# Performance work log

Hardware: AMD Instinct MI355X
Metric: run time of the kernel (lower is better)

Reference implementation:

```python
import jax, jax.numpy as jnp
import numpy as np

B, S, D, H = 8, 1024, 512, 8
HD = D // H
EPS = 1e-5


def layer_norm(x, g, b):
    m = jnp.mean(x, axis=-1, keepdims=True)
    v = jnp.mean(jnp.square(x - m), axis=-1, keepdims=True)
    return (x - m) * jax.lax.rsqrt(v + EPS) * g + b


def mha(x, w_in, b_in, w_out, b_out):
    # x: [B,S,D]; w_in: [3D,D]; PyTorch MultiheadAttention math (no dropout, eval)
    b, s, d = x.shape
    qkv = x @ w_in.T + b_in                      # [B,S,3D]
    q, k, v = jnp.split(qkv, 3, axis=-1)
    q = q.reshape(b, s, H, HD)
    k = k.reshape(b, s, H, HD)
    v = v.reshape(b, s, H, HD)
    scores = jnp.einsum('bqhd,bkhd->bhqk', q, k) / np.sqrt(HD)
    a = jax.nn.softmax(scores, axis=-1)
    o = jnp.einsum('bhqk,bkhd->bqhd', a, v).reshape(b, s, d)
    return o @ w_out.T + b_out


def interp_linear(y, out_size):
    # y: [B,S_in,D]; torch F.interpolate(mode='linear', align_corners=False)
    s_in = y.shape[1]
    scale = s_in / out_size
    src = (jnp.arange(out_size, dtype=jnp.float32) + 0.5) * scale - 0.5
    src = jnp.clip(src, 0.0, s_in - 1.0)
    i0 = jnp.floor(src).astype(jnp.int32)
    i1 = jnp.minimum(i0 + 1, s_in - 1)
    w = (src - i0.astype(jnp.float32))[None, :, None]
    return y[:, i0, :] * (1.0 - w) + y[:, i1, :] * w


def setup_inputs() -> dict:
    key = jax.random.key(0)
    ks = jax.random.split(key, 16)
    sd = 0.02
    return {
        'x': jax.random.normal(ks[0], (B, S, D), jnp.float32),
        'w_in1': jax.random.normal(ks[1], (3 * D, D), jnp.float32) * sd,
        'b_in1': jnp.zeros((3 * D,), jnp.float32),
        'w_out1': jax.random.normal(ks[2], (D, D), jnp.float32) * sd,
        'b_out1': jnp.zeros((D,), jnp.float32),
        'w_in2': jax.random.normal(ks[3], (3 * D, D), jnp.float32) * sd,
        'b_in2': jnp.zeros((3 * D,), jnp.float32),
        'w_out2': jax.random.normal(ks[4], (D, D), jnp.float32) * sd,
        'b_out2': jnp.zeros((D,), jnp.float32),
        'g1': jnp.ones((D,), jnp.float32), 'beta1': jnp.zeros((D,), jnp.float32),
        'g2': jnp.ones((D,), jnp.float32), 'beta2': jnp.zeros((D,), jnp.float32),
        'g3': jnp.ones((D,), jnp.float32), 'beta3': jnp.zeros((D,), jnp.float32),
        'w_ff1': jax.random.normal(ks[5], (4 * D, D), jnp.float32) * sd,
        'b_ff1': jnp.zeros((4 * D,), jnp.float32),
        'w_ff2': jax.random.normal(ks[6], (D, 4 * D), jnp.float32) * sd,
        'b_ff2': jnp.zeros((D,), jnp.float32),
    }


def reference(x, w_in1, b_in1, w_out1, b_out1, w_in2, b_in2, w_out2, b_out2,
              g1, beta1, g2, beta2, g3, beta3, w_ff1, b_ff1, w_ff2, b_ff2):
    a1 = mha(x, w_in1, b_in1, w_out1, b_out1)
    x = layer_norm(x + a1, g1, beta1)
    # avg_pool1d kernel=2 stride=2 ceil_mode (S even -> exact halving)
    pooled = x.reshape(B, S // 2, 2, D).mean(axis=2)
    a2 = mha(pooled, w_in2, b_in2, w_out2, b_out2)
    up = interp_linear(a2, S)
    x = layer_norm(x + up, g2, beta2)
    h = jax.nn.gelu(x @ w_ff1.T + b_ff1, approximate=False)
    ff = h @ w_ff2.T + b_ff2
    return layer_norm(x + ff, g3, beta3)
```

## Files before the change

kernel.cpp:

```cpp
#include <hip/hip_runtime.h>
#include <hip/hip_bf16.h>
#include <math.h>

typedef __hip_bfloat16 bf16;
typedef __attribute__((ext_vector_type(8))) short short8;
typedef __attribute__((ext_vector_type(4))) float f32x4;

__device__ __forceinline__ float ldf(const float* p, size_t i) { return p[i]; }
__device__ __forceinline__ float ldf(const bf16*  p, size_t i) { return __bfloat162float(p[i]); }
__device__ __forceinline__ void  stf(float* p, size_t i, float v) { p[i] = v; }
__device__ __forceinline__ void  stf(bf16*  p, size_t i, float v) { p[i] = __float2bfloat16(v); }

__global__ __launch_bounds__(256) void cvt_kernel(
    const float* __restrict__ src, bf16* __restrict__ dst, int n)
{
    for (int i = blockIdx.x * 256 + threadIdx.x; i < n; i += gridDim.x * 256)
        dst[i] = __float2bfloat16(src[i]);
}

template <int EPI>
__global__ __launch_bounds__(256) void gemm_mfma(
    const bf16* __restrict__ A, const bf16* __restrict__ W,
    const float* __restrict__ bias, bf16* __restrict__ C,
    int M, int N, int K)
{
    constexpr int LP = 72;
    __shared__ __align__(16) bf16 Asl[128 * LP];
    __shared__ __align__(16) bf16 Bsl[128 * LP];

    const int tid  = threadIdx.x;
    const int lane = tid & 63;
    const int wave = tid >> 6;
    const int wm   = wave >> 1;
    const int wn   = wave & 1;
    const int l15  = lane & 15;
    const int quad = lane >> 4;

    const int row0 = blockIdx.y * 128, col0 = blockIdx.x * 128;

    f32x4 acc[4][4] = {};

    for (int k0 = 0; k0 < K; k0 += 64) {
        #pragma unroll
        for (int t = 0; t < 4; t++) {
            int chunk = tid + 256 * t;
            int r = chunk >> 3, c = (chunk & 7) * 8;
            *(short8*)&Asl[r * LP + c] =
                *(const short8*)&A[(size_t)(row0 + r) * K + k0 + c];
            *(short8*)&Bsl[r * LP + c] =
                *(const short8*)&W[(size_t)(col0 + r) * K + k0 + c];
        }
        __syncthreads();

        #pragma unroll
        for (int ks = 0; ks < 64; ks += 32) {
            short8 af[4], bfr[4];
            #pragma unroll
            for (int mt = 0; mt < 4; mt++)
                af[mt] = *(const short8*)&Asl[(wm * 64 + mt * 16 + l15) * LP + ks + quad * 8];
            #pragma unroll
            for (int nt = 0; nt < 4; nt++)
                bfr[nt] = *(const short8*)&Bsl[(wn * 64 + nt * 16 + l15) * LP + ks + quad * 8];
            #pragma unroll
            for (int mt = 0; mt < 4; mt++)
                #pragma unroll
                for (int nt = 0; nt < 4; nt++)
                    acc[mt][nt] = __builtin_amdgcn_mfma_f32_16x16x32_bf16(
                        af[mt], bfr[nt], acc[mt][nt], 0, 0, 0);
        }
        __syncthreads();
    }

    #pragma unroll
    for (int mt = 0; mt < 4; mt++) {
        int row = row0 + wm * 64 + mt * 16 + quad * 4;
        #pragma unroll
        for (int nt = 0; nt < 4; nt++) {
            int col = col0 + wn * 64 + nt * 16 + l15;
            float bv = bias[col];
            #pragma unroll
            for (int r = 0; r < 4; r++) {
                float v = acc[mt][nt][r] + bv;
                if (EPI == 1) v = 0.5f * v * (1.0f + erff(v * 0.70710678118654752f));
                C[(size_t)(row + r) * N + col] = __float2bfloat16(v);
            }
        }
    }
}

__global__ __launch_bounds__(256) void flash_attn_mfma(
    const bf16* __restrict__ qkv, bf16* __restrict__ o, int S)
{
    __shared__ __align__(16) bf16 Ks[64 * 72];
    __shared__ __align__(16) bf16 Vt[64 * 68];
    __shared__ __align__(16) bf16 Pl[4][16 * 72];
    __shared__ float aX[4][16];

    const int tid = threadIdx.x;
    const int wave = tid >> 6, lane = tid & 63;
    const int l15 = lane & 15, quad = lane >> 4;
    const int q0 = blockIdx.x * 64, h = blockIdx.y, bb = blockIdx.z;
    const bf16* base = qkv + (size_t)bb * S * 1536 + h * 64;

    const size_t qoff = (size_t)(q0 + wave * 16 + l15) * 1536;
    short8 qf0 = *(const short8*)&base[qoff + quad * 8];
    short8 qf1 = *(const short8*)&base[qoff + 32 + quad * 8];

    f32x4 oacc[4] = {};
    float mrow = -3.0e38f, lrow = 0.f;

    for (int k0 = 0; k0 < S; k0 += 64) {
        __syncthreads();

        #pragma unroll
        for (int t = 0; t < 2; t++) {
            int c = tid + 256 * t;
            int r = c >> 3, col = (c & 7) * 8;
            *(short8*)&Ks[r * 72 + col] =
                *(const short8*)&base[(size_t)(k0 + r) * 1536 + 512 + col];
        }
        #pragma unroll
        for (int i = 0; i < 16; i++) {
            int r = i * 4 + wave;
            Vt[lane * 68 + r] = base[(size_t)(k0 + r) * 1536 + 1024 + lane];
        }
        __syncthreads();

        f32x4 st[4] = {};
        #pragma unroll
        for (int mt = 0; mt < 4; mt++) {
            short8 kf0 = *(const short8*)&Ks[(mt * 16 + l15) * 72 + quad * 8];
            short8 kf1 = *(const short8*)&Ks[(mt * 16 + l15) * 72 + 32 + quad * 8];
            st[mt] = __builtin_amdgcn_mfma_f32_16x16x32_bf16(kf0, qf0, st[mt], 0, 0, 0);
            st[mt] = __builtin_amdgcn_mfma_f32_16x16x32_bf16(kf1, qf1, st[mt], 0, 0, 0);
        }

        float cm = -3.0e38f;
        #pragma unroll
        for (int mt = 0; mt < 4; mt++)
            #pragma unroll
            for (int r = 0; r < 4; r++) {
                st[mt][r] *= 0.125f;
                cm = fmaxf(cm, st[mt][r]);
            }
        cm = fmaxf(cm, __shfl_xor(cm, 16));
        cm = fmaxf(cm, __shfl_xor(cm, 32));
        float mn = fmaxf(mrow, cm);
        float alpha = __expf(mrow - mn);
        mrow = mn;

        float ps = 0.f;
        #pragma unroll
        for (int mt = 0; mt < 4; mt++)
            #pragma unroll
            for (int r = 0; r < 4; r++) {
                float p = __expf(st[mt][r] - mn);
                ps += p;
                Pl[wave][l15 * 72 + mt * 16 + quad * 4 + r] = __float2bfloat16(p);
            }
        ps += __shfl_xor(ps, 16);
        ps += __shfl_xor(ps, 32);
        lrow = lrow * alpha + ps;

        if (quad == 0) aX[wave][l15] = alpha;
        float a4[4];
        #pragma unroll
        for (int r = 0; r < 4; r++) a4[r] = aX[wave][quad * 4 + r];
        #pragma unroll
        for (int nt = 0; nt < 4; nt++)
            #pragma unroll
            for (int r = 0; r < 4; r++) oacc[nt][r] *= a4[r];

        #pragma unroll
        for (int kb = 0; kb < 2; kb++) {
            short8 pf = *(const short8*)&Pl[wave][l15 * 72 + kb * 32 + quad * 8];
            #pragma unroll
            for (int nt = 0; nt < 4; nt++) {
                const bf16* vp = &Vt[(nt * 16 + l15) * 68 + kb * 32 + quad * 8];
                short8 vf;
                *(long*)&vf = *(const long*)vp;
                *((long*)&vf + 1) = *(const long*)(vp + 4);
                oacc[nt] = __builtin_amdgcn_mfma_f32_16x16x32_bf16(pf, vf, oacc[nt], 0, 0, 0);
            }
        }
    }

    if (quad == 0) aX[wave][l15] = 1.0f / lrow;
    float iv[4];
    #pragma unroll
    for (int r = 0; r < 4; r++) iv[r] = aX[wave][quad * 4 + r];

    #pragma unroll
    for (int nt = 0; nt < 4; nt++)
        #pragma unroll
        for (int r = 0; r < 4; r++) {
            size_t row = (size_t)bb * S + q0 + wave * 16 + quad * 4 + r;
            o[row * 512 + h * 64 + nt * 16 + l15] = __float2bfloat16(oacc[nt][r] * iv[r]);
        }
}

template <typename AT, typename OT, bool INTERP>
__global__ __launch_bounds__(256) void ln_kernel(
    const AT* __restrict__ a, const bf16* __restrict__ bsrc,
    const float* __restrict__ g, const float* __restrict__ beta,
    OT* __restrict__ out)
{
    const int row = blockIdx.x;
    const int t = threadIdx.x;
    const size_t base = (size_t)row * 512;

    float a0 = ldf(a, base + t), a1 = ldf(a, base + t + 256);
    float b0, b1;
    if (INTERP) {
        int s = row & 1023, bb = row >> 10;
        float src = fminf(fmaxf((s + 0.5f) * 0.5f - 0.5f, 0.f), 511.f);
        int i0 = (int)src;
        int i1 = min(i0 + 1, 511);
        float w = src - (float)i0;
        size_t r0 = ((size_t)bb * 512 + i0) * 512;
        size_t r1 = ((size_t)bb * 512 + i1) * 512;
        b0 = __bfloat162float(bsrc[r0 + t]) * (1.f - w) + __bfloat162float(bsrc[r1 + t]) * w;
        b1 = __bfloat162float(bsrc[r0 + t + 256]) * (1.f - w) + __bfloat162float(bsrc[r1 + t + 256]) * w;
    } else {
        b0 = __bfloat162float(bsrc[base + t]);
        b1 = __bfloat162float(bsrc[base + t + 256]);
    }
    float v0 = a0 + b0, v1 = a1 + b1;

    __shared__ float red[4];
    const int lane = t & 63, wid = t >> 6;

    float sm = v0 + v1;
    #pragma unroll
    for (int off = 32; off > 0; off >>= 1) sm += __shfl_xor(sm, off);
    if (lane == 0) red[wid] = sm;
    __syncthreads();
    sm = red[0] + red[1] + red[2] + red[3];
    const float mean = sm * (1.0f / 512.0f);

    float d0 = v0 - mean, d1 = v1 - mean;
    float vv = d0 * d0 + d1 * d1;
    __syncthreads();
    #pragma unroll
    for (int off = 32; off > 0; off >>= 1) vv += __shfl_xor(vv, off);
    if (lane == 0) red[wid] = vv;
    __syncthreads();
    vv = red[0] + red[1] + red[2] + red[3];
    const float rstd = rsqrtf(vv * (1.0f / 512.0f) + 1e-5f);

    stf(out, base + t,       d0 * rstd * g[t]       + beta[t]);
    stf(out, base + t + 256, d1 * rstd * g[t + 256] + beta[t + 256]);
}

__global__ __launch_bounds__(256) void pool_kernel(
    const bf16* __restrict__ x, bf16* __restrict__ p)
{
    size_t i = (size_t)blockIdx.x * 256 + threadIdx.x;
    size_t d = i & 511;
    size_t rs = i >> 9;
    size_t b = rs >> 9, s = rs & 511;
    size_t r = (b * 1024 + 2 * s) * 512 + d;
    p[i] = __float2bfloat16(0.5f * (__bfloat162float(x[r]) + __bfloat162float(x[r + 512])));
}

extern "C" void kernel_launch(void* const* d_in, const int* in_sizes, int n_in,
                              void* d_out, int out_size, void* d_ws, size_t ws_size,
                              hipStream_t stream)
{
    const float* x      = (const float*)d_in[0];
    const float* w_in1  = (const float*)d_in[1];
    const float* b_in1  = (const float*)d_in[2];
    const float* w_out1 = (const float*)d_in[3];
    const float* b_out1 = (const float*)d_in[4];
    const float* w_in2  = (const float*)d_in[5];
    const float* b_in2  = (const float*)d_in[6];
    const float* w_out2 = (const float*)d_in[7];
    const float* b_out2 = (const float*)d_in[8];
    const float* g1     = (const float*)d_in[9];
    const float* be1    = (const float*)d_in[10];
    const float* g2     = (const float*)d_in[11];
    const float* be2    = (const float*)d_in[12];
    const float* g3     = (const float*)d_in[13];
    const float* be3    = (const float*)d_in[14];
    const float* w_ff1  = (const float*)d_in[15];
    const float* b_ff1  = (const float*)d_in[16];
    const float* w_ff2  = (const float*)d_in[17];
    const float* b_ff2  = (const float*)d_in[18];

    bf16* ws     = (bf16*)d_ws;
    bf16* xb     = ws + 0;
    bf16* wq1    = ws + 4194304;
    bf16* wo1    = ws + 4980736;
    bf16* wq2    = ws + 5242880;
    bf16* wo2    = ws + 6029312;
    bf16* wf1    = ws + 6291456;
    bf16* wf2    = ws + 7340032;
    bf16* qkv1   = ws + 8388608;
    bf16* o1     = ws + 20971520;
    bf16* a1     = ws + 25165824;
    bf16* x1     = ws + 29360128;
    bf16* pooled = ws + 33554432;
    bf16* qkv2   = ws + 35651584;
    bf16* o2     = ws + 41943040;
    bf16* a2     = ws + 44040192;
    bf16* x2     = ws + 46137344;
    bf16* h      = ws + 8388608;
    bf16* ff     = ws + 25165824;

    dim3 blk(256);

    cvt_kernel<<<1024, blk, 0, stream>>>(x, xb, 4194304);
    cvt_kernel<<<512, blk, 0, stream>>>(w_in1, wq1, 786432);
    cvt_kernel<<<256, blk, 0, stream>>>(w_out1, wo1, 262144);
    cvt_kernel<<<512, blk, 0, stream>>>(w_in2, wq2, 786432);
    cvt_kernel<<<256, blk, 0, stream>>>(w_out2, wo2, 262144);
    cvt_kernel<<<512, blk, 0, stream>>>(w_ff1, wf1, 1048576);
    cvt_kernel<<<512, blk, 0, stream>>>(w_ff2, wf2, 1048576);

    gemm_mfma<0><<<dim3(12, 64), blk, 0, stream>>>(xb, wq1, b_in1, qkv1, 8192, 1536, 512);
    flash_attn_mfma<<<dim3(16, 8, 8), blk, 0, stream>>>(qkv1, o1, 1024);
    gemm_mfma<0><<<dim3(4, 64), blk, 0, stream>>>(o1, wo1, b_out1, a1, 8192, 512, 512);
    ln_kernel<float, bf16, false><<<8192, blk, 0, stream>>>(x, a1, g1, be1, x1);
    pool_kernel<<<8192, blk, 0, stream>>>(x1, pooled);
    gemm_mfma<0><<<dim3(12, 32), blk, 0, stream>>>(pooled, wq2, b_in2, qkv2, 4096, 1536, 512);
    flash_attn_mfma<<<dim3(8, 8, 8), blk, 0, stream>>>(qkv2, o2, 512);
    gemm_mfma<0><<<dim3(4, 32), blk, 0, stream>>>(o2, wo2, b_out2, a2, 4096, 512, 512);
    ln_kernel<bf16, bf16, true><<<8192, blk, 0, stream>>>(x1, a2, g2, be2, x2);
    gemm_mfma<1><<<dim3(16, 64), blk, 0, stream>>>(x2, wf1, b_ff1, h, 8192, 2048, 512);
    gemm_mfma<0><<<dim3(4, 64), blk, 0, stream>>>(h, wf2, b_ff2, ff, 8192, 512, 2048);
    ln_kernel<bf16, float, false><<<8192, blk, 0, stream>>>(x2, ff, g3, be3, (float*)d_out);
}
```

Baseline: 370.0 us.

## Use direct global-to-LDS loads in GEMM, multi-tile flash attention, fuse weight conversions

The GEMM now loads A/W tiles straight into shared memory with global_load_lds, drops the LDS row padding and moves the barrier to the top of the loop. Flash attention is templated to process two 16-row Q tiles per wave, reusing K/V fragments across them, and switches to exp2 with a folded scale, packed V transpose stores and vectorized P writes. The six weight conversions are merged into one launch. The unpadded LDS layout may cause bank conflicts on the MFMA fragment reads, and the larger attention tile halves the grid for the first attention.

```diff
diff --git a/kernel.cpp b/kernel.cpp
--- a/kernel.cpp
+++ b/kernel.cpp
@@ -4,6 +4,7 @@
 
 typedef __hip_bfloat16 bf16;
 typedef __attribute__((ext_vector_type(8))) short short8;
+typedef __attribute__((ext_vector_type(4))) short s4v;
 typedef __attribute__((ext_vector_type(4))) float f32x4;
 
 __device__ __forceinline__ float ldf(const float* p, size_t i) { return p[i]; }
@@ -11,11 +12,36 @@
 __device__ __forceinline__ void  stf(float* p, size_t i, float v) { p[i] = v; }
 __device__ __forceinline__ void  stf(bf16*  p, size_t i, float v) { p[i] = __float2bfloat16(v); }
 
+__device__ __forceinline__ float ex2(float x) { return __builtin_amdgcn_exp2f(x); }
+
+__device__ __forceinline__ void gl16(const void* gp, void* lp) {
+    __builtin_amdgcn_global_load_lds(
+        (const __attribute__((address_space(1))) void*)gp,
+        (__attribute__((address_space(3))) void*)lp, 16, 0, 0);
+}
+
 __global__ __launch_bounds__(256) void cvt_kernel(
     const float* __restrict__ src, bf16* __restrict__ dst, int n)
 {
     for (int i = blockIdx.x * 256 + threadIdx.x; i < n; i += gridDim.x * 256)
         dst[i] = __float2bfloat16(src[i]);
+}
+
+__global__ __launch_bounds__(256) void cvt_w(
+    const float* __restrict__ s0, const float* __restrict__ s1,
+    const float* __restrict__ s2, const float* __restrict__ s3,
+    const float* __restrict__ s4, const float* __restrict__ s5,
+    bf16* __restrict__ dst)
+{
+    int i = blockIdx.x * 256 + threadIdx.x;
+    const float* s; int off;
+    if      (i <  786432) { s = s0; off = 0; }
+    else if (i < 1048576) { s = s1; off =  786432; }
+    else if (i < 1835008) { s = s2; off = 1048576; }
+    else if (i < 2097152) { s = s3; off = 1835008; }
+    else if (i < 3145728) { s = s4; off = 2097152; }
+    else                  { s = s5; off = 3145728; }
+    dst[i] = __float2bfloat16(s[i - off]);
 }
 
 template <int EPI>
@@ -24,9 +50,8 @@
     const float* __restrict__ bias, bf16* __restrict__ C,
     int M, int N, int K)
 {
-    constexpr int LP = 72;
-    __shared__ __align__(16) bf16 Asl[128 * LP];
-    __shared__ __align__(16) bf16 Bsl[128 * LP];
+    __shared__ __align__(16) bf16 Asl[128 * 64];
+    __shared__ __align__(16) bf16 Bsl[128 * 64];
 
     const int tid  = threadIdx.x;
     const int lane = tid & 63;
@@ -35,20 +60,21 @@
     const int wn   = wave & 1;
     const int l15  = lane & 15;
     const int quad = lane >> 4;
+    const int sr   = lane >> 3;
+    const int sc   = (lane & 7) * 8;
 
     const int row0 = blockIdx.y * 128, col0 = blockIdx.x * 128;
 
     f32x4 acc[4][4] = {};
 
     for (int k0 = 0; k0 < K; k0 += 64) {
+        __syncthreads();
         #pragma unroll
         for (int t = 0; t < 4; t++) {
-            int chunk = tid + 256 * t;
-            int r = chunk >> 3, c = (chunk & 7) * 8;
-            *(short8*)&Asl[r * LP + c] =
-                *(const short8*)&A[(size_t)(row0 + r) * K + k0 + c];
-            *(short8*)&Bsl[r * LP + c] =
-                *(const short8*)&W[(size_t)(col0 + r) * K + k0 + c];
+            int r0 = wave * 32 + t * 8;
+            int r  = r0 + sr;
+            gl16(&A[(size_t)(row0 + r) * K + k0 + sc], &Asl[r0 * 64]);
+            gl16(&W[(size_t)(col0 + r) * K + k0 + sc], &Bsl[r0 * 64]);
         }
         __syncthreads();
 
@@ -57,10 +83,10 @@
             short8 af[4], bfr[4];
             #pragma unroll
             for (int mt = 0; mt < 4; mt++)
-                af[mt] = *(const short8*)&Asl[(wm * 64 + mt * 16 + l15) * LP + ks + quad * 8];
+                af[mt] = *(const short8*)&Asl[(wm * 64 + mt * 16 + l15) * 64 + ks + quad * 8];
             #pragma unroll
             for (int nt = 0; nt < 4; nt++)
-                bfr[nt] = *(const short8*)&Bsl[(wn * 64 + nt * 16 + l15) * LP + ks + quad * 8];
+                bfr[nt] = *(const short8*)&Bsl[(wn * 64 + nt * 16 + l15) * 64 + ks + quad * 8];
             #pragma unroll
             for (int mt = 0; mt < 4; mt++)
                 #pragma unroll
@@ -68,7 +94,6 @@
                     acc[mt][nt] = __builtin_amdgcn_mfma_f32_16x16x32_bf16(
                         af[mt], bfr[nt], acc[mt][nt], 0, 0, 0);
         }
-        __syncthreads();
     }
 
     #pragma unroll
@@ -88,26 +113,35 @@
     }
 }
 
+template <int NS>
 __global__ __launch_bounds__(256) void flash_attn_mfma(
     const bf16* __restrict__ qkv, bf16* __restrict__ o, int S)
 {
     __shared__ __align__(16) bf16 Ks[64 * 72];
     __shared__ __align__(16) bf16 Vt[64 * 68];
-    __shared__ __align__(16) bf16 Pl[4][16 * 72];
-    __shared__ float aX[4][16];
+    __shared__ __align__(16) bf16 Pl[4][NS * 16 * 72];
+    __shared__ float aX[4][NS * 16];
 
     const int tid = threadIdx.x;
     const int wave = tid >> 6, lane = tid & 63;
     const int l15 = lane & 15, quad = lane >> 4;
-    const int q0 = blockIdx.x * 64, h = blockIdx.y, bb = blockIdx.z;
+    const int q0 = blockIdx.x * (64 * NS), h = blockIdx.y, bb = blockIdx.z;
     const bf16* base = qkv + (size_t)bb * S * 1536 + h * 64;
 
-    const size_t qoff = (size_t)(q0 + wave * 16 + l15) * 1536;
-    short8 qf0 = *(const short8*)&base[qoff + quad * 8];
-    short8 qf1 = *(const short8*)&base[qoff + 32 + quad * 8];
-
-    f32x4 oacc[4] = {};
-    float mrow = -3.0e38f, lrow = 0.f;
+    short8 qf[NS][2];
+    #pragma unroll
+    for (int s = 0; s < NS; s++) {
+        size_t qoff = (size_t)(q0 + (wave * NS + s) * 16 + l15) * 1536;
+        qf[s][0] = *(const short8*)&base[qoff + quad * 8];
+        qf[s][1] = *(const short8*)&base[qoff + 32 + quad * 8];
+    }
+
+    f32x4 oacc[NS][4] = {};
+    float mrow[NS], lrow[NS];
+    #pragma unroll
+    for (int s = 0; s < NS; s++) { mrow[s] = -3.0e38f; lrow[s] = 0.f; }
+
+    const float CE = 0.18033688f;
 
     for (int k0 = 0; k0 < S; k0 += 64) {
         __syncthreads();
@@ -120,83 +154,106 @@
                 *(const short8*)&base[(size_t)(k0 + r) * 1536 + 512 + col];
         }
         #pragma unroll
-        for (int i = 0; i < 16; i++) {
-            int r = i * 4 + wave;
-            Vt[lane * 68 + r] = base[(size_t)(k0 + r) * 1536 + 1024 + lane];
+        for (int i = 0; i < 8; i++) {
+            int r = (wave * 8 + i) * 2;
+            union { bf16 b[2]; unsigned u; } pk;
+            pk.b[0] = base[(size_t)(k0 + r) * 1536 + 1024 + lane];
+            pk.b[1] = base[(size_t)(k0 + r + 1) * 1536 + 1024 + lane];
+            *(unsigned*)&Vt[lane * 68 + r] = pk.u;
         }
         __syncthreads();
 
-        f32x4 st[4] = {};
+        f32x4 st[NS][4] = {};
         #pragma unroll
         for (int mt = 0; mt < 4; mt++) {
             short8 kf0 = *(const short8*)&Ks[(mt * 16 + l15) * 72 + quad * 8];
             short8 kf1 = *(const short8*)&Ks[(mt * 16 + l15) * 72 + 32 + quad * 8];
-            st[mt] = __builtin_amdgcn_mfma_f32_16x16x32_bf16(kf0, qf0, st[mt], 0, 0, 0);
-            st[mt] = __builtin_amdgcn_mfma_f32_16x16x32_bf16(kf1, qf1, st[mt], 0, 0, 0);
-        }
-
-        float cm = -3.0e38f;
-        #pragma unroll
-        for (int mt = 0; mt < 4; mt++)
-            #pragma unroll
-            for (int r = 0; r < 4; r++) {
-                st[mt][r] *= 0.125f;
-                cm = fmaxf(cm, st[mt][r]);
-            }
-        cm = fmaxf(cm, __shfl_xor(cm, 16));
-        cm = fmaxf(cm, __shfl_xor(cm, 32));
-        float mn = fmaxf(mrow, cm);
-        float alpha = __expf(mrow - mn);
-        mrow = mn;
-
-        float ps = 0.f;
-        #pragma unroll
-        for (int mt = 0; mt < 4; mt++)
-            #pragma unroll
-            for (int r = 0; r < 4; r++) {
-                float p = __expf(st[mt][r] - mn);
-                ps += p;
-                Pl[wave][l15 * 72 + mt * 16 + quad * 4 + r] = __float2bfloat16(p);
-            }
-        ps += __shfl_xor(ps, 16);
-        ps += __shfl_xor(ps, 32);
-        lrow = lrow * alpha + ps;
-
-        if (quad == 0) aX[wave][l15] = alpha;
-        float a4[4];
-        #pragma unroll
-        for (int r = 0; r < 4; r++) a4[r] = aX[wave][quad * 4 + r];
-        #pragma unroll
-        for (int nt = 0; nt < 4; nt++)
-            #pragma unroll
-            for (int r = 0; r < 4; r++) oacc[nt][r] *= a4[r];
+            #pragma unroll
+            for (int s = 0; s < NS; s++) {
+                st[s][mt] = __builtin_amdgcn_mfma_f32_16x16x32_bf16(kf0, qf[s][0], st[s][mt], 0, 0, 0);
+                st[s][mt] = __builtin_amdgcn_mfma_f32_16x16x32_bf16(kf1, qf[s][1], st[s][mt], 0, 0, 0);
+            }
+        }
+
+        #pragma unroll
+        for (int s = 0; s < NS; s++) {
+            float cm = -3.0e38f;
+            #pragma unroll
+            for (int mt = 0; mt < 4; mt++)
+                #pragma unroll
+                for (int r = 0; r < 4; r++) cm = fmaxf(cm, st[s][mt][r]);
+            cm = fmaxf(cm, __shfl_xor(cm, 16));
+            cm = fmaxf(cm, __shfl_xor(cm, 32));
+            float mn = fmaxf(mrow[s], cm);
+            float alpha = ex2((mrow[s] - mn) * CE);
+            mrow[s] = mn;
+            float mb = mn * CE;
+            float ps = 0.f;
+            #pragma unroll
+            for (int mt = 0; mt < 4; mt++) {
+                s4v pw;
+                #pragma unroll
+                for (int r = 0; r < 4; r++) {
+                    float p = ex2(st[s][mt][r] * CE - mb);
+                    ps += p;
+                    union { bf16 b; short h; } cv;
+                    cv.b = __float2bfloat16(p);
+                    pw[r] = cv.h;
+                }
+                *(s4v*)&Pl[wave][(s * 16 + l15) * 72 + mt * 16 + quad * 4] = pw;
+            }
+            ps += __shfl_xor(ps, 16);
+            ps += __shfl_xor(ps, 32);
+            lrow[s] = lrow[s] * alpha + ps;
+            if (quad == 0) aX[wave][s * 16 + l15] = alpha;
+        }
+
+        #pragma unroll
+        for (int s = 0; s < NS; s++) {
+            float a4[4];
+            #pragma unroll
+            for (int r = 0; r < 4; r++) a4[r] = aX[wave][s * 16 + quad * 4 + r];
+            #pragma unroll
+            for (int nt = 0; nt < 4; nt++)
+                #pragma unroll
+                for (int r = 0; r < 4; r++) oacc[s][nt][r] *= a4[r];
+        }
 
         #pragma unroll
         for (int kb = 0; kb < 2; kb++) {
-            short8 pf = *(const short8*)&Pl[wave][l15 * 72 + kb * 32 + quad * 8];
+            short8 pf[NS];
+            #pragma unroll
+            for (int s = 0; s < NS; s++)
+                pf[s] = *(const short8*)&Pl[wave][(s * 16 + l15) * 72 + kb * 32 + quad * 8];
             #pragma unroll
             for (int nt = 0; nt < 4; nt++) {
                 const bf16* vp = &Vt[(nt * 16 + l15) * 68 + kb * 32 + quad * 8];
                 short8 vf;
                 *(long*)&vf = *(const long*)vp;
                 *((long*)&vf + 1) = *(const long*)(vp + 4);
-                oacc[nt] = __builtin_amdgcn_mfma_f32_16x16x32_bf16(pf, vf, oacc[nt], 0, 0, 0);
-            }
-        }
-    }
-
-    if (quad == 0) aX[wave][l15] = 1.0f / lrow;
-    float iv[4];
-    #pragma unroll
-    for (int r = 0; r < 4; r++) iv[r] = aX[wave][quad * 4 + r];
-
-    #pragma unroll
-    for (int nt = 0; nt < 4; nt++)
-        #pragma unroll
-        for (int r = 0; r < 4; r++) {
-            size_t row = (size_t)bb * S + q0 + wave * 16 + quad * 4 + r;
-            o[row * 512 + h * 64 + nt * 16 + l15] = __float2bfloat16(oacc[nt][r] * iv[r]);
-        }
+                #pragma unroll
+                for (int s = 0; s < NS; s++)
+                    oacc[s][nt] = __builtin_amdgcn_mfma_f32_16x16x32_bf16(pf[s], vf, oacc[s][nt], 0, 0, 0);
+            }
+        }
+    }
+
+    #pragma unroll
+    for (int s = 0; s < NS; s++)
+        if (quad == 0) aX[wave][s * 16 + l15] = 1.0f / lrow[s];
+    #pragma unroll
+    for (int s = 0; s < NS; s++) {
+        float iv[4];
+        #pragma unroll
+        for (int r = 0; r < 4; r++) iv[r] = aX[wave][s * 16 + quad * 4 + r];
+        #pragma unroll
+        for (int nt = 0; nt < 4; nt++)
+            #pragma unroll
+            for (int r = 0; r < 4; r++) {
+                size_t row = (size_t)bb * S + q0 + (wave * NS + s) * 16 + quad * 4 + r;
+                o[row * 512 + h * 64 + nt * 16 + l15] = __float2bfloat16(oacc[s][nt][r] * iv[r]);
+            }
+    }
 }
 
 template <typename AT, typename OT, bool INTERP>
@@ -309,21 +366,16 @@
 
     dim3 blk(256);
 
-    cvt_kernel<<<1024, blk, 0, stream>>>(x, xb, 4194304);
-    cvt_kernel<<<512, blk, 0, stream>>>(w_in1, wq1, 786432);
-    cvt_kernel<<<256, blk, 0, stream>>>(w_out1, wo1, 262144);
-    cvt_kernel<<<512, blk, 0, stream>>>(w_in2, wq2, 786432);
-    cvt_kernel<<<256, blk, 0, stream>>>(w_out2, wo2, 262144);
-    cvt_kernel<<<512, blk, 0, stream>>>(w_ff1, wf1, 1048576);
-    cvt_kernel<<<512, blk, 0, stream>>>(w_ff2, wf2, 1048576);
+    cvt_kernel<<<4096, blk, 0, stream>>>(x, xb, 4194304);
+    cvt_w<<<16384, blk, 0, stream>>>(w_in1, w_out1, w_in2, w_out2, w_ff1, w_ff2, wq1);
 
     gemm_mfma<0><<<dim3(12, 64), blk, 0, stream>>>(xb, wq1, b_in1, qkv1, 8192, 1536, 512);
-    flash_attn_mfma<<<dim3(16, 8, 8), blk, 0, stream>>>(qkv1, o1, 1024);
+    flash_attn_mfma<2><<<dim3(8, 8, 8), blk, 0, stream>>>(qkv1, o1, 1024);
     gemm_mfma<0><<<dim3(4, 64), blk, 0, stream>>>(o1, wo1, b_out1, a1, 8192, 512, 512);
     ln_kernel<float, bf16, false><<<8192, blk, 0, stream>>>(x, a1, g1, be1, x1);
     pool_kernel<<<8192, blk, 0, stream>>>(x1, pooled);
     gemm_mfma<0><<<dim3(12, 32), blk, 0, stream>>>(pooled, wq2, b_in2, qkv2, 4096, 1536, 512);
-    flash_attn_mfma<<<dim3(8, 8, 8), blk, 0, stream>>>(qkv2, o2, 512);
+    flash_attn_mfma<1><<<dim3(8, 8, 8), blk, 0, stream>>>(qkv2, o2, 512);
     gemm_mfma<0><<<dim3(4, 32), blk, 0, stream>>>(o2, wo2, b_out2, a2, 4096, 512, 512);
     ln_kernel<bf16, bf16, true><<<8192, blk, 0, stream>>>(x1, a2, g2, be2, x2);
     gemm_mfma<1><<<dim3(16, 64), blk, 0, stream>>>(x2, wf1, b_ff1, h, 8192, 2048, 512);
```

After: 366.9 us. About the same (-0.9%).
